# Kernel tuning notes

Measured on AMD Instinct MI355X. Metric: run time of the kernel, lower is better.

## Reference

```python
import jax, jax.numpy as jnp
from jax import lax
import numpy as np

U = 128  # num_units
F = 64   # input features
OUT = 6  # dense head units


def _lstm_layer(x, W, R, b):
    """Keras-style LSTM (gate order i,f,g,o; sigmoid recurrent act, tanh act).
    x: [B,T,D], W: [D,4U], R: [U,4U], b: [4U]. Returns (all_h [B,T,U], last_h [B,U])."""
    B = x.shape[0]
    xw = jnp.einsum('btd,dk->btk', x, W) + b  # precompute input projection [B,T,4U]

    def step(carry, xw_t):
        h, c = carry
        z = xw_t + h @ R  # [B,4U]
        i, f, g, o = jnp.split(z, 4, axis=-1)
        i = jax.nn.sigmoid(i)
        f = jax.nn.sigmoid(f)
        g = jnp.tanh(g)
        o = jax.nn.sigmoid(o)
        c = f * c + i * g
        h = o * jnp.tanh(c)
        return (h, c), h

    h0 = jnp.zeros((B, U), dtype=x.dtype)
    c0 = jnp.zeros((B, U), dtype=x.dtype)
    (h_last, _), hs = lax.scan(step, (h0, c0), jnp.swapaxes(xw, 0, 1))
    return jnp.swapaxes(hs, 0, 1), h_last


def setup_inputs() -> dict:
    key = jax.random.key(0)
    ks = jax.random.split(key, 12)
    s = 0.05
    inp = {
        'x': jax.random.normal(ks[0], (256, 512, F), dtype=jnp.float32),
        'W0': jax.random.normal(ks[1], (F, 4 * U), dtype=jnp.float32) * s,
        'R0': jax.random.normal(ks[2], (U, 4 * U), dtype=jnp.float32) * s,
        'b0': jnp.zeros((4 * U,), dtype=jnp.float32),
        'W1': jax.random.normal(ks[3], (U, 4 * U), dtype=jnp.float32) * s,
        'R1': jax.random.normal(ks[4], (U, 4 * U), dtype=jnp.float32) * s,
        'b1': jnp.zeros((4 * U,), dtype=jnp.float32),
        'W2': jax.random.normal(ks[5], (U, 4 * U), dtype=jnp.float32) * s,
        'R2': jax.random.normal(ks[6], (U, 4 * U), dtype=jnp.float32) * s,
        'b2': jnp.zeros((4 * U,), dtype=jnp.float32),
        'Wd': jax.random.normal(ks[7], (U, OUT), dtype=jnp.float32) * s,
        'bd': jnp.zeros((OUT,), dtype=jnp.float32),
    }
    return inp


def reference(x, W0, R0, b0, W1, R1, b1, W2, R2, b2, Wd, bd):
    h, _ = _lstm_layer(x, W0, R0, b0)      # [B,T,U]
    h, _ = _lstm_layer(h, W1, R1, b1)      # [B,T,U]
    _, h_last = _lstm_layer(h, W2, R2, b2) # [B,U] (return_sequences=False)
    return h_last @ Wd + bd                # [B,6]
```

## Files before the change

### kernel.cpp

```cpp
#include <hip/hip_runtime.h>
#include <cstdint>
#include <cstddef>

#define U4    512
#define UNITS 128
#define BATCH 256
#define TSEQ  512
#define FEAT  64
#define SEQS  8
#define NBLK  (BATCH / SEQS)

typedef short short8 __attribute__((ext_vector_type(8)));
typedef float f32x4  __attribute__((ext_vector_type(4)));
typedef unsigned short tab_t[16][136];

#define MFMA_BF16(C, A, B) \
    asm("v_mfma_f32_16x16x32_bf16 %0, %1, %2, %0" : "+v"(C) : "v"(A), "a"(B))

__device__ __forceinline__ void barrier_lds_only() {
    __builtin_amdgcn_sched_barrier(0);
    asm volatile("s_waitcnt lgkmcnt(0)" ::: "memory");
    __builtin_amdgcn_s_barrier();
    __builtin_amdgcn_sched_barrier(0);
}

__device__ __forceinline__ float sigm(float x) {
    float e = __expf(-x);
    return __fdividef(1.0f, 1.0f + e);
}
__device__ __forceinline__ float tanh_fast(float x) {
    float e = __expf(2.0f * x);
    return 1.0f - __fdividef(2.0f, e + 1.0f);
}

__device__ __forceinline__ unsigned short f2bf(float f) {
    unsigned u = __float_as_uint(f);
    unsigned r = u + 0x7FFFu + ((u >> 16) & 1u);
    return (unsigned short)(r >> 16);
}
__device__ __forceinline__ float bf2f(unsigned short h) {
    return __uint_as_float(((unsigned)h) << 16);
}

__global__ __launch_bounds__(256)
void rw_frag(const float* __restrict__ R0, const float* __restrict__ R1,
             const float* __restrict__ R2,
             const float* __restrict__ W0, const float* __restrict__ W1,
             const float* __restrict__ W2,
             unsigned short* __restrict__ Rf, unsigned short* __restrict__ Wf)
{
    if (blockIdx.x < 192) {
        int gid = blockIdx.x * 256 + threadIdx.x;
        int l    = gid >> 14;
        int r    = gid & 16383;
        int lane = r & 63;
        int fi   = r >> 6;
        int pass = fi & 1;
        int kt   = (fi >> 1) & 3;
        int gate = (fi >> 3) & 3;
        int w    = fi >> 5;
        const float* R = (l == 0) ? R0 : (l == 1) ? R1 : R2;

        int col = gate * UNITS + w * 16 + (lane & 15);
        int k0  = kt * 32 + (lane >> 4) * 8;
        short8 v;
        #pragma unroll
        for (int j = 0; j < 8; ++j) {
            float x = R[(size_t)(k0 + j) * U4 + col];
            unsigned short hi = f2bf(x);
            unsigned short s = pass ? f2bf(x - bf2f(hi)) : hi;
            v[j] = (short)s;
        }
        *(short8*)(Rf + (size_t)gid * 8) = v;
    } else {
        int gid = (blockIdx.x - 192) * 256 + threadIdx.x;
        int l    = gid >> 14;
        int r    = gid & 16383;
        int lane = r & 63;
        int fi   = r >> 6;
        int pass = fi & 1;
        int kt   = (fi >> 1) & 3;
        int nt   = fi >> 3;
        const float* W = (l == 0) ? W0 : (l == 1) ? W1 : W2;
        const int K = (l == 0) ? FEAT : UNITS;

        int col = nt * 16 + (lane & 15);
        int k0  = kt * 32 + (lane >> 4) * 8;
        short8 v;
        #pragma unroll
        for (int j = 0; j < 8; ++j) {
            float x = (k0 + j < K) ? W[(size_t)(k0 + j) * U4 + col] : 0.f;
            unsigned short hi = f2bf(x);
            unsigned short s = pass ? f2bf(x - bf2f(hi)) : hi;
            v[j] = (short)s;
        }
        *(short8*)(Wf + (size_t)gid * 8) = v;
    }
}

struct PCell {
    const void* in;
    float* out;
    const unsigned short* wf;
    const float* bias;
    int sB, sT, t0, K, packed, pad_;
};
struct PStage { PCell c[2]; };

__device__ __forceinline__ void proj_body(const PCell& ce, int bx, int tcShift,
                                          tab_t* __restrict__ atab)
{
    const int tid  = threadIdx.x;
    const int lane = tid & 63;
    const int w    = tid >> 6;
    const int m    = lane & 15;
    const int quad = lane >> 4;
    const int TcMask = (1 << tcShift) - 1;
    const int m0 = bx * 64;

    short8 bf[4][4][2];
    #pragma unroll
    for (int nt = 0; nt < 4; ++nt)
        #pragma unroll
        for (int kt = 0; kt < 4; ++kt)
            #pragma unroll
            for (int pp = 0; pp < 2; ++pp)
                bf[nt][kt][pp] = *(const short8*)(
                    ce.wf + ((size_t)((((w * 4 + nt) * 4 + kt) * 2) + pp) * 64 + lane) * 8);

    if (ce.packed) {
        const unsigned int* __restrict__ inp = (const unsigned int*)ce.in;
        #pragma unroll
        for (int rep = 0; rep < 16; ++rep) {
            int idx = rep * 512 + tid;
            int row = idx >> 7;
            int k   = idx & 127;
            int rg  = m0 + row;
            int b = rg >> tcShift, tc = rg & TcMask;
            unsigned int u = inp[(size_t)b * ce.sB + (size_t)(ce.t0 + tc) * ce.sT + k];
            atab[row >> 3][2 * (row & 7)][k]     = (unsigned short)(u & 0xFFFFu);
            atab[row >> 3][2 * (row & 7) + 1][k] = (unsigned short)(u >> 16);
        }
    } else {
        const float* __restrict__ inp = (const float*)ce.in;
        #pragma unroll
        for (int rep = 0; rep < 16; ++rep) {
            int idx = rep * 512 + tid;
            int row = idx >> 7;
            int k   = idx & 127;
            int rg  = m0 + row;
            int b = rg >> tcShift, tc = rg & TcMask;
            float x = 0.f;
            if (k < ce.K)
                x = inp[(size_t)b * ce.sB + (size_t)(ce.t0 + tc) * ce.sT + k];
            unsigned short hi = f2bf(x);
            atab[row >> 3][2 * (row & 7)][k]     = hi;
            atab[row >> 3][2 * (row & 7) + 1][k] = f2bf(x - bf2f(hi));
        }
    }
    __syncthreads();

    float bb[4];
    #pragma unroll
    for (int nt = 0; nt < 4; ++nt) bb[nt] = ce.bias[w * 64 + nt * 16 + m];

    float* __restrict__ outp = ce.out;
    #pragma unroll 1
    for (int r = 0; r < 8; ++r) {
        short8 af[4];
        #pragma unroll
        for (int kt = 0; kt < 4; ++kt)
            af[kt] = *(const short8*)(&atab[r][m][kt * 32 + quad * 8]);

        f32x4 C[4];
        #pragma unroll
        for (int nt = 0; nt < 4; ++nt) C[nt] = f32x4{0.f, 0.f, 0.f, 0.f};

        #pragma unroll
        for (int kt = 0; kt < 4; ++kt)
            #pragma unroll
            for (int pp = 0; pp < 2; ++pp)
                #pragma unroll
                for (int nt = 0; nt < 4; ++nt)
                    MFMA_BF16(C[nt], af[kt], bf[nt][kt][pp]);

        int row0 = m0 + r * 8 + 2 * quad;
        #pragma unroll
        for (int nt = 0; nt < 4; ++nt) {
            float z0 = C[nt].x + C[nt].y + bb[nt];
            float z1 = C[nt].z + C[nt].w + bb[nt];
            int col = w * 64 + nt * 16 + m;
            outp[(size_t)row0 * U4 + col]       = z0;
            outp[(size_t)(row0 + 1) * U4 + col] = z1;
        }
    }
}

__global__ __launch_bounds__(512, 2)
void proj_mfma(PStage ps, int tcShift)
{
    __shared__ __align__(16) unsigned short smem[8 * 16 * 136];
    proj_body(ps.c[blockIdx.y], blockIdx.x, tcShift, (tab_t*)smem);
}

struct Cell {
    const float* xw;
    const unsigned short* rf;
    float* hs;
    float* cs;
    unsigned int* hout;
    int init;
    int pad_;
};

__device__ __forceinline__ void lstm_body(const Cell& ce, int blk, int Tc,
                                          tab_t* __restrict__ htab)
{
    const float* __restrict__ xw = ce.xw;
    const unsigned short* __restrict__ Rf = ce.rf;
    float* __restrict__ h_state = ce.hs;
    float* __restrict__ c_state = ce.cs;
    unsigned int* __restrict__ h_out = ce.hout;
    const int init = ce.init;

    const int tid  = threadIdx.x;
    const int lane = tid & 63;
    const int w    = tid >> 6;
    const int m    = lane & 15;
    const int quad = lane >> 4;

    short8 bf[4][4][2];
    #pragma unroll
    for (int g = 0; g < 4; ++g)
        #pragma unroll
        for (int kt = 0; kt < 4; ++kt)
            #pragma unroll
            for (int pp = 0; pp < 2; ++pp)
                bf[g][kt][pp] = *(const short8*)(
                    Rf + ((size_t)((((w * 4 + g) * 4 + kt) * 2) + pp) * 64 + lane) * 8);

    const int unit = w * 16 + m;
    const int s0   = 2 * quad;
    const int s1   = s0 + 1;

    float c0 = 0.f, c1 = 0.f;
    if (!init) {
        c0 = c_state[(blk * SEQS + s0) * UNITS + unit];
        c1 = c_state[(blk * SEQS + s1) * UNITS + unit];
    }
    {
        int uu = tid & 127;
        #pragma unroll
        for (int i = 0; i < 2; ++i) {
            int s = (tid >> 7) + i * 4;
            float hv = init ? 0.f : h_state[(blk * SEQS + s) * UNITS + uu];
            unsigned short hi = f2bf(hv);
            htab[0][2 * s][uu]     = hi;
            htab[0][2 * s + 1][uu] = f2bf(hv - bf2f(hi));
        }
    }
    __syncthreads();

    const float* xw0 = xw + (size_t)(blk * SEQS + s0) * Tc * U4 + unit;
    const float* xw1 = xw + (size_t)(blk * SEQS + s1) * Tc * U4 + unit;

    float xa[8], xb[8];
    #pragma unroll
    for (int g = 0; g < 4; ++g) {
        xa[g]     = xw0[g * UNITS];
        xa[4 + g] = xw1[g * UNITS];
    }
    {
        const size_t o1 = (size_t)((Tc > 1) ? 1 : 0) * U4;
        #pragma unroll
        for (int g = 0; g < 4; ++g) {
            xb[g]     = xw0[o1 + g * UNITS];
            xb[4 + g] = xw1[o1 + g * UNITS];
        }
    }

    float hl0 = 0.f, hl1 = 0.f;

    auto STEP = [&](int t, int p, float (&xc)[8]) {
        short8 af[4];
        #pragma unroll
        for (int kt = 0; kt < 4; ++kt)
            af[kt] = *(const short8*)(&htab[p][m][kt * 32 + quad * 8]);

        f32x4 C0 = {xc[0], 0.f, xc[4], 0.f};
        f32x4 C1 = {xc[1], 0.f, xc[5], 0.f};
        f32x4 C2 = {xc[2], 0.f, xc[6], 0.f};
        f32x4 C3 = {xc[3], 0.f, xc[7], 0.f};

        int tp = t + 2; if (tp >= Tc) tp = Tc - 1;
        const size_t off = (size_t)tp * U4;
        #pragma unroll
        for (int g = 0; g < 4; ++g) {
            xc[g]     = xw0[off + g * UNITS];
            xc[4 + g] = xw1[off + g * UNITS];
        }

        __builtin_amdgcn_s_setprio(1);
        #pragma unroll
        for (int kt = 0; kt < 4; ++kt) {
            #pragma unroll
            for (int pp = 0; pp < 2; ++pp) {
                MFMA_BF16(C0, af[kt], bf[0][kt][pp]);
                MFMA_BF16(C1, af[kt], bf[1][kt][pp]);
            }
        }
        float zi0 = C0.x + C0.y, zi1 = C0.z + C0.w;
        float zf0 = C1.x + C1.y, zf1 = C1.z + C1.w;
        float iv0 = sigm(zi0), iv1 = sigm(zi1);
        float fv0 = sigm(zf0), fv1 = sigm(zf1);

        #pragma unroll
        for (int kt = 0; kt < 4; ++kt) {
            #pragma unroll
            for (int pp = 0; pp < 2; ++pp) {
                MFMA_BF16(C2, af[kt], bf[2][kt][pp]);
                MFMA_BF16(C3, af[kt], bf[3][kt][pp]);
            }
        }
        __builtin_amdgcn_s_setprio(0);

        float zg0 = C2.x + C2.y, zg1 = C2.z + C2.w;
        float zo0 = C3.x + C3.y, zo1 = C3.z + C3.w;

        float gv0 = tanh_fast(zg0), ov0 = sigm(zo0);
        c0 = __builtin_fmaf(fv0, c0, iv0 * gv0);
        float hv0 = ov0 * tanh_fast(c0);

        float gv1 = tanh_fast(zg1), ov1 = sigm(zo1);
        c1 = __builtin_fmaf(fv1, c1, iv1 * gv1);
        float hv1 = ov1 * tanh_fast(c1);

        hl0 = hv0; hl1 = hv1;

        unsigned short hi0 = f2bf(hv0);
        unsigned short lo0 = f2bf(hv0 - bf2f(hi0));
        htab[p ^ 1][4 * quad + 0][unit] = hi0;
        htab[p ^ 1][4 * quad + 1][unit] = lo0;
        unsigned short hi1 = f2bf(hv1);
        unsigned short lo1 = f2bf(hv1 - bf2f(hi1));
        htab[p ^ 1][4 * quad + 2][unit] = hi1;
        htab[p ^ 1][4 * quad + 3][unit] = lo1;

        if (h_out) {
            h_out[((size_t)(blk * SEQS + s0) * Tc + t) * UNITS + unit] =
                (unsigned int)hi0 | ((unsigned int)lo0 << 16);
            h_out[((size_t)(blk * SEQS + s1) * Tc + t) * UNITS + unit] =
                (unsigned int)hi1 | ((unsigned int)lo1 << 16);
        }
        barrier_lds_only();
    };

    #pragma unroll 1
    for (int t = 0; t < Tc; t += 2) {
        STEP(t,     0, xa);
        STEP(t + 1, 1, xb);
    }

    c_state[(blk * SEQS + s0) * UNITS + unit] = c0;
    c_state[(blk * SEQS + s1) * UNITS + unit] = c1;
    h_state[(blk * SEQS + s0) * UNITS + unit] = hl0;
    h_state[(blk * SEQS + s1) * UNITS + unit] = hl1;
}

struct FusedArgs {
    Cell lc[3];
    PCell pc;
    int n_lstm;
    int has_proj;
};

__global__ __launch_bounds__(512, 2)
void stage_fused(FusedArgs fa, int Tc, int tcShift)
{
    __shared__ __align__(16) unsigned short smem[8 * 16 * 136];
    int bx = blockIdx.x;
    if (bx < fa.n_lstm * NBLK)
        lstm_body(fa.lc[bx >> 5], bx & 31, Tc, (tab_t*)smem);
    else
        proj_body(fa.pc, bx - fa.n_lstm * NBLK, tcShift, (tab_t*)smem);
}

__global__ __launch_bounds__(256)
void dense_head(const float* __restrict__ h2, const float* __restrict__ Wd,
                const float* __restrict__ bd, float* __restrict__ out)
{
    int b = threadIdx.x;
    float acc[6];
    #pragma unroll
    for (int o = 0; o < 6; ++o) acc[o] = bd[o];
    #pragma unroll 4
    for (int k = 0; k < UNITS; ++k) {
        float hv = h2[b * UNITS + k];
        #pragma unroll
        for (int o = 0; o < 6; ++o)
            acc[o] = __builtin_fmaf(hv, Wd[k * 6 + o], acc[o]);
    }
    #pragma unroll
    for (int o = 0; o < 6; ++o) out[b * 6 + o] = acc[o];
}

extern "C" void kernel_launch(void* const* d_in, const int* in_sizes, int n_in,
                              void* d_out, int out_size, void* d_ws, size_t ws_size,
                              hipStream_t stream)
{
    (void)in_sizes; (void)n_in; (void)out_size;
    const float* x  = (const float*)d_in[0];
    const float* Ws[3] = {(const float*)d_in[1], (const float*)d_in[4], (const float*)d_in[7]};
    const float* Rs[3] = {(const float*)d_in[2], (const float*)d_in[5], (const float*)d_in[8]};
    const float* bs[3] = {(const float*)d_in[3], (const float*)d_in[6], (const float*)d_in[9]};
    const float* Wd = (const float*)d_in[10];
    const float* bd = (const float*)d_in[11];
    float* out = (float*)d_out;

    int tcShift = 6;
    while (tcShift > 2) {
        size_t need = ((size_t)1 << tcShift) * 2359296u + 2359296u;
        if (need <= ws_size) break;
        --tcShift;
    }
    const int Tc = 1 << tcShift;
    const int nCh = TSEQ / Tc;
    const int projGrid = BATCH * Tc / 64;

    const size_t xwStride = (size_t)BATCH * Tc * U4;
    const size_t hcStride = (size_t)BATCH * Tc * UNITS;

    float* xw = (float*)d_ws;
    unsigned int* hc = (unsigned int*)(xw + 4 * xwStride);
    float* hs = (float*)(hc + 2 * hcStride);
    float* cs = hs + 3 * BATCH * UNITS;
    unsigned short* Rf = (unsigned short*)(cs + 3 * BATCH * UNITS);
    unsigned short* Wf = Rf + 3 * 131072;

    rw_frag<<<384, 256, 0, stream>>>(Rs[0], Rs[1], Rs[2], Ws[0], Ws[1], Ws[2], Rf, Wf);

    {
        PStage ps{};
        ps.c[0].in = x; ps.c[0].out = xw; ps.c[0].wf = Wf; ps.c[0].bias = bs[0];
        ps.c[0].sB = TSEQ * FEAT; ps.c[0].sT = FEAT; ps.c[0].t0 = 0;
        ps.c[0].K = FEAT; ps.c[0].packed = 0;
        proj_mfma<<<dim3(projGrid, 1), 512, 0, stream>>>(ps, tcShift);
    }

    for (int s = 0; s <= nCh + 1; ++s) {
        int lo = s - (nCh - 1); if (lo < 0) lo = 0;
        int hi = (s < 2) ? s : 2;
        if (lo > hi) continue;

        PStage ps{};
        int pn = 0;
        int plo = (lo > 1) ? lo : 1;
        for (int lam = plo; lam <= hi; ++lam) {
            ps.c[pn].in   = hc + (size_t)(lam - 1) * hcStride;
            ps.c[pn].out  = xw + (size_t)(1 + lam) * xwStride;
            ps.c[pn].wf   = Wf + (size_t)lam * 131072;
            ps.c[pn].bias = bs[lam];
            ps.c[pn].sB   = Tc * UNITS;
            ps.c[pn].sT   = UNITS;
            ps.c[pn].t0   = 0;
            ps.c[pn].K    = UNITS;
            ps.c[pn].packed = 1;
            ++pn;
        }
        if (pn) proj_mfma<<<dim3(projGrid, pn), 512, 0, stream>>>(ps, tcShift);

        FusedArgs fa{};
        int n = 0;
        for (int lam = lo; lam <= hi; ++lam) {
            int c = s - lam;
            fa.lc[n].xw   = (lam == 0) ? xw + (size_t)(c & 1) * xwStride
                                       : xw + (size_t)(1 + lam) * xwStride;
            fa.lc[n].rf   = Rf + (size_t)lam * 131072;
            fa.lc[n].hs   = hs + lam * BATCH * UNITS;
            fa.lc[n].cs   = cs + lam * BATCH * UNITS;
            fa.lc[n].hout = (lam < 2) ? (hc + (size_t)lam * hcStride) : nullptr;
            fa.lc[n].init = (c == 0) ? 1 : 0;
            ++n;
        }
        fa.n_lstm = n;
        int c0 = s + 1;
        fa.has_proj = (c0 <= nCh - 1) ? 1 : 0;
        if (fa.has_proj) {
            fa.pc.in = x; fa.pc.out = xw + (size_t)(c0 & 1) * xwStride;
            fa.pc.wf = Wf; fa.pc.bias = bs[0];
            fa.pc.sB = TSEQ * FEAT; fa.pc.sT = FEAT; fa.pc.t0 = c0 * Tc;
            fa.pc.K = FEAT; fa.pc.packed = 0;
        }
        int gridx = n * NBLK + (fa.has_proj ? projGrid : 0);
        stage_fused<<<dim3(gridx), 512, 0, stream>>>(fa, Tc, tcShift);
    }

    dense_head<<<1, 256, 0, stream>>>(hs + 2 * BATCH * UNITS, Wd, bd, out);
}
```

Baseline: 1.119 ms.

## Fold layer input projections into fused stage kernel with atomic-counter dependencies

Removes the separate per-stage proj_mfma launch for layers 1 and 2 and runs those projection blocks inside stage_fused, placed first in the grid. LSTM blocks spin on an agent-scope atomic counter until every projection block for their layer has finished. To keep this safe, the hc buffers become double-buffered by chunk parity. The aim is to cut one kernel launch and its gap per stage and to overlap the projection with other work, at the cost of spin-waiting blocks, which relies on the projection blocks being scheduled first, plus extra workspace.

```diff
diff --git a/kernel.cpp b/kernel.cpp
--- a/kernel.cpp
+++ b/kernel.cpp
@@ -47,8 +47,11 @@
              const float* __restrict__ R2,
              const float* __restrict__ W0, const float* __restrict__ W1,
              const float* __restrict__ W2,
-             unsigned short* __restrict__ Rf, unsigned short* __restrict__ Wf)
-{
+             unsigned short* __restrict__ Rf, unsigned short* __restrict__ Wf,
+             unsigned int* __restrict__ ctrs)
+{
+    if (blockIdx.x == 0 && threadIdx.x < 64) ctrs[threadIdx.x] = 0;
+
     if (blockIdx.x < 192) {
         int gid = blockIdx.x * 256 + threadIdx.x;
         int l    = gid >> 14;
@@ -103,9 +106,10 @@
     float* out;
     const unsigned short* wf;
     const float* bias;
+    unsigned int* doneCtr;
     int sB, sT, t0, K, packed, pad_;
 };
-struct PStage { PCell c[2]; };
+struct PStage { PCell c[1]; };
 
 __device__ __forceinline__ void proj_body(const PCell& ce, int bx, int tcShift,
                                           tab_t* __restrict__ atab)
@@ -194,13 +198,21 @@
             outp[(size_t)(row0 + 1) * U4 + col] = z1;
         }
     }
+
+    if (ce.doneCtr) {
+        __threadfence();
+        __syncthreads();
+        if (threadIdx.x == 0)
+            __hip_atomic_fetch_add(ce.doneCtr, 1u, __ATOMIC_RELEASE,
+                                   __HIP_MEMORY_SCOPE_AGENT);
+    }
 }
 
 __global__ __launch_bounds__(512, 2)
 void proj_mfma(PStage ps, int tcShift)
 {
     __shared__ __align__(16) unsigned short smem[8 * 16 * 136];
-    proj_body(ps.c[blockIdx.y], blockIdx.x, tcShift, (tab_t*)smem);
+    proj_body(ps.c[0], blockIdx.x, tcShift, (tab_t*)smem);
 }
 
 struct Cell {
@@ -209,13 +221,20 @@
     float* hs;
     float* cs;
     unsigned int* hout;
+    unsigned int* waitCtr;
+    unsigned int waitTarget;
     int init;
-    int pad_;
 };
 
 __device__ __forceinline__ void lstm_body(const Cell& ce, int blk, int Tc,
                                           tab_t* __restrict__ htab)
 {
+    if (ce.waitTarget) {
+        while (__hip_atomic_load(ce.waitCtr, __ATOMIC_ACQUIRE,
+                                 __HIP_MEMORY_SCOPE_AGENT) < ce.waitTarget)
+            __builtin_amdgcn_s_sleep(2);
+    }
+
     const float* __restrict__ xw = ce.xw;
     const unsigned short* __restrict__ Rf = ce.rf;
     float* __restrict__ h_state = ce.hs;
@@ -368,21 +387,28 @@
 }
 
 struct FusedArgs {
-    Cell lc[3];
+    Cell  lc[3];
+    PCell pl[2];
     PCell pc;
-    int n_lstm;
-    int has_proj;
+    int n_lstm, n_projL, has_proj0, pad_;
 };
 
 __global__ __launch_bounds__(512, 2)
-void stage_fused(FusedArgs fa, int Tc, int tcShift)
+void stage_fused(FusedArgs fa, int Tc, int tcShift, int pg)
 {
     __shared__ __align__(16) unsigned short smem[8 * 16 * 136];
     int bx = blockIdx.x;
-    if (bx < fa.n_lstm * NBLK)
-        lstm_body(fa.lc[bx >> 5], bx & 31, Tc, (tab_t*)smem);
-    else
-        proj_body(fa.pc, bx - fa.n_lstm * NBLK, tcShift, (tab_t*)smem);
+    int npl = fa.n_projL * pg;
+    if (bx < npl) {
+        proj_body(fa.pl[bx / pg], bx % pg, tcShift, (tab_t*)smem);
+        return;
+    }
+    bx -= npl;
+    if (fa.has_proj0) {
+        if (bx < pg) { proj_body(fa.pc, bx, tcShift, (tab_t*)smem); return; }
+        bx -= pg;
+    }
+    lstm_body(fa.lc[bx >> 5], bx & 31, Tc, (tab_t*)smem);
 }
 
 __global__ __launch_bounds__(256)
@@ -419,7 +445,7 @@
 
     int tcShift = 6;
     while (tcShift > 2) {
-        size_t need = ((size_t)1 << tcShift) * 2359296u + 2359296u;
+        size_t need = ((size_t)1 << tcShift) * 2621440u + 2359552u;
         if (need <= ws_size) break;
         --tcShift;
     }
@@ -432,19 +458,22 @@
 
     float* xw = (float*)d_ws;
     unsigned int* hc = (unsigned int*)(xw + 4 * xwStride);
-    float* hs = (float*)(hc + 2 * hcStride);
+    float* hs = (float*)(hc + 4 * hcStride);
     float* cs = hs + 3 * BATCH * UNITS;
     unsigned short* Rf = (unsigned short*)(cs + 3 * BATCH * UNITS);
     unsigned short* Wf = Rf + 3 * 131072;
-
-    rw_frag<<<384, 256, 0, stream>>>(Rs[0], Rs[1], Rs[2], Ws[0], Ws[1], Ws[2], Rf, Wf);
+    unsigned int* ctrs = (unsigned int*)(Wf + 3 * 131072);
+
+    rw_frag<<<384, 256, 0, stream>>>(Rs[0], Rs[1], Rs[2], Ws[0], Ws[1], Ws[2],
+                                     Rf, Wf, ctrs);
 
     {
         PStage ps{};
         ps.c[0].in = x; ps.c[0].out = xw; ps.c[0].wf = Wf; ps.c[0].bias = bs[0];
+        ps.c[0].doneCtr = nullptr;
         ps.c[0].sB = TSEQ * FEAT; ps.c[0].sT = FEAT; ps.c[0].t0 = 0;
         ps.c[0].K = FEAT; ps.c[0].packed = 0;
-        proj_mfma<<<dim3(projGrid, 1), 512, 0, stream>>>(ps, tcShift);
+        proj_mfma<<<dim3(projGrid), 512, 0, stream>>>(ps, tcShift);
     }
 
     for (int s = 0; s <= nCh + 1; ++s) {
@@ -452,24 +481,26 @@
         int hi = (s < 2) ? s : 2;
         if (lo > hi) continue;
 
-        PStage ps{};
+        FusedArgs fa{};
+
         int pn = 0;
         int plo = (lo > 1) ? lo : 1;
         for (int lam = plo; lam <= hi; ++lam) {
-            ps.c[pn].in   = hc + (size_t)(lam - 1) * hcStride;
-            ps.c[pn].out  = xw + (size_t)(1 + lam) * xwStride;
-            ps.c[pn].wf   = Wf + (size_t)lam * 131072;
-            ps.c[pn].bias = bs[lam];
-            ps.c[pn].sB   = Tc * UNITS;
-            ps.c[pn].sT   = UNITS;
-            ps.c[pn].t0   = 0;
-            ps.c[pn].K    = UNITS;
-            ps.c[pn].packed = 1;
+            int c = s - lam;
+            fa.pl[pn].in      = hc + (size_t)((lam - 1) * 2 + (c & 1)) * hcStride;
+            fa.pl[pn].out     = xw + (size_t)(1 + lam) * xwStride;
+            fa.pl[pn].wf      = Wf + (size_t)lam * 131072;
+            fa.pl[pn].bias    = bs[lam];
+            fa.pl[pn].doneCtr = ctrs + (s * 2 + (lam - 1));
+            fa.pl[pn].sB      = Tc * UNITS;
+            fa.pl[pn].sT      = UNITS;
+            fa.pl[pn].t0      = 0;
+            fa.pl[pn].K       = UNITS;
+            fa.pl[pn].packed  = 1;
             ++pn;
         }
-        if (pn) proj_mfma<<<dim3(projGrid, pn), 512, 0, stream>>>(ps, tcShift);
-
-        FusedArgs fa{};
+        fa.n_projL = pn;
+
         int n = 0;
         for (int lam = lo; lam <= hi; ++lam) {
             int c = s - lam;
@@ -478,21 +509,26 @@
             fa.lc[n].rf   = Rf + (size_t)lam * 131072;
             fa.lc[n].hs   = hs + lam * BATCH * UNITS;
             fa.lc[n].cs   = cs + lam * BATCH * UNITS;
-            fa.lc[n].hout = (lam < 2) ? (hc + (size_t)lam * hcStride) : nullptr;
+            fa.lc[n].hout = (lam < 2)
+                ? (hc + (size_t)(lam * 2 + (c & 1)) * hcStride) : nullptr;
+            fa.lc[n].waitCtr    = (lam >= 1) ? (ctrs + (s * 2 + (lam - 1))) : nullptr;
+            fa.lc[n].waitTarget = (lam >= 1) ? (unsigned int)projGrid : 0u;
             fa.lc[n].init = (c == 0) ? 1 : 0;
             ++n;
         }
         fa.n_lstm = n;
+
         int c0 = s + 1;
-        fa.has_proj = (c0 <= nCh - 1) ? 1 : 0;
-        if (fa.has_proj) {
+        fa.has_proj0 = (c0 <= nCh - 1) ? 1 : 0;
+        if (fa.has_proj0) {
             fa.pc.in = x; fa.pc.out = xw + (size_t)(c0 & 1) * xwStride;
-            fa.pc.wf = Wf; fa.pc.bias = bs[0];
+            fa.pc.wf = Wf; fa.pc.bias = bs[0]; fa.pc.doneCtr = nullptr;
             fa.pc.sB = TSEQ * FEAT; fa.pc.sT = FEAT; fa.pc.t0 = c0 * Tc;
             fa.pc.K = FEAT; fa.pc.packed = 0;
         }
-        int gridx = n * NBLK + (fa.has_proj ? projGrid : 0);
-        stage_fused<<<dim3(gridx), 512, 0, stream>>>(fa, Tc, tcShift);
+
+        int gridx = pn * projGrid + (fa.has_proj0 ? projGrid : 0) + n * NBLK;
+        stage_fused<<<dim3(gridx), 512, 0, stream>>>(fa, Tc, tcShift, projGrid);
     }
 
     dense_head<<<1, 256, 0, stream>>>(hs + 2 * BATCH * UNITS, Wd, bd, out);
```

New measurement: 2.347 ms. 110% more time.
